# Performance work log

Hardware: AMD Instinct MI355X
Metric: run time of the kernel (lower is better)

The kernel has to match this reference:

```python
import jax, jax.numpy as jnp
import numpy as np

LEAK = 0.2
NUM_GRAPHS = 64


def _gat(h_in, src, dst, eh, W, att_src, att_dst, att_edge, lin_edge_W, bias, N):
    # PyG GATConv with edge_dim, concat=False (mean over heads)
    H, C = att_src.shape
    h = (h_in @ W).reshape(N, H, C)                      # [N,H,C]
    e = (eh @ lin_edge_W).reshape(-1, H, C)              # [Eaug,H,C]
    a_s = jnp.einsum('nhc,hc->nh', h, att_src)           # [N,H]
    a_d = jnp.einsum('nhc,hc->nh', h, att_dst)
    a_e = jnp.einsum('ehc,hc->eh', e, att_edge)          # [Eaug,H]
    score = jax.nn.leaky_relu(a_s[src] + a_d[dst] + a_e, LEAK)
    # scatter-softmax over incoming edges of each destination node
    m = jax.ops.segment_max(score, dst, num_segments=N)
    ex = jnp.exp(score - m[dst])
    den = jax.ops.segment_sum(ex, dst, num_segments=N)
    alpha = ex / den[dst]                                # [Eaug,H]
    out = jax.ops.segment_sum(alpha[:, :, None] * h[src], dst, num_segments=N)
    return out.mean(axis=1) + bias                       # concat=False -> head mean


def setup_inputs() -> dict:
    key = jax.random.key(0)
    ks = jax.random.split(key, 32)
    N, E, F, FE, HID, H, NT = 30000, 480000, 64, 16, 64, 4, 16
    Cin1 = F + HID
    s = 0.05
    d = {
        'x': jax.random.normal(ks[0], (N, F), jnp.float32),
        'edge_attr': jax.random.normal(ks[1], (E, FE), jnp.float32),
        'node_emb': jax.random.normal(ks[2], (NT, HID), jnp.float32) * s,
        'edge_W': jax.random.normal(ks[3], (FE, HID), jnp.float32) * s,
        'edge_b': jnp.zeros((HID,), jnp.float32),
        'W1': jax.random.normal(ks[4], (Cin1, H * HID), jnp.float32) * s,
        'as1': jax.random.normal(ks[5], (H, HID), jnp.float32) * s,
        'ad1': jax.random.normal(ks[6], (H, HID), jnp.float32) * s,
        'ae1': jax.random.normal(ks[7], (H, HID), jnp.float32) * s,
        'leW1': jax.random.normal(ks[8], (HID, H * HID), jnp.float32) * s,
        'b1': jnp.zeros((HID,), jnp.float32),
        'W2': jax.random.normal(ks[9], (HID, H * HID), jnp.float32) * s,
        'as2': jax.random.normal(ks[10], (H, HID), jnp.float32) * s,
        'ad2': jax.random.normal(ks[11], (H, HID), jnp.float32) * s,
        'ae2': jax.random.normal(ks[12], (H, HID), jnp.float32) * s,
        'leW2': jax.random.normal(ks[13], (HID, H * HID), jnp.float32) * s,
        'b2': jnp.zeros((HID,), jnp.float32),
        'sage_Wl': jax.random.normal(ks[14], (HID, HID), jnp.float32) * s,
        'sage_bl': jnp.zeros((HID,), jnp.float32),
        'sage_Wr': jax.random.normal(ks[15], (HID, HID), jnp.float32) * s,
        'lin1_W': jax.random.normal(ks[16], (HID, HID), jnp.float32) * s,
        'lin1_b': jnp.zeros((HID,), jnp.float32),
        'lin2_W': jax.random.normal(ks[17], (HID, HID), jnp.float32) * s,
        'lin2_b': jnp.zeros((HID,), jnp.float32),
        'tel_W': jax.random.normal(ks[18], (HID, 1), jnp.float32) * s,
        'tel_b': jnp.zeros((1,), jnp.float32),
        'comp_W': jax.random.normal(ks[19], (HID, 1), jnp.float32) * s,
        'comp_b': jnp.zeros((1,), jnp.float32),
        'pch_W': jax.random.normal(ks[20], (HID, 1), jnp.float32) * s,
        'pch_b': jnp.zeros((1,), jnp.float32),
        'edge_index': jax.random.randint(ks[21], (2, E), 0, N, jnp.int32),
        'batch': jnp.sort(jax.random.randint(ks[22], (N,), 0, NUM_GRAPHS, jnp.int32)),
        'node_type': jax.random.randint(ks[23], (N,), 0, NT, jnp.int32),
    }
    return d


def reference(x, edge_attr, node_emb, edge_W, edge_b,
              W1, as1, ad1, ae1, leW1, b1,
              W2, as2, ad2, ae2, leW2, b2,
              sage_Wl, sage_bl, sage_Wr,
              lin1_W, lin1_b, lin2_W, lin2_b,
              tel_W, tel_b, comp_W, comp_b, pch_W, pch_b,
              edge_index, batch, node_type):
    N = x.shape[0]
    src0, dst0 = edge_index[0], edge_index[1]

    h0 = jnp.concatenate([x, node_emb[node_type]], axis=-1)   # [N, F+HID]
    eh = edge_attr @ edge_W + edge_b                          # [E, HID]

    # GATConv default add_self_loops=True, fill_value='mean' on edge_attr
    loop = jnp.arange(N, dtype=src0.dtype)
    src = jnp.concatenate([src0, loop])
    dst = jnp.concatenate([dst0, loop])
    eh_aug = jnp.concatenate([eh, jnp.broadcast_to(eh.mean(axis=0), (N, eh.shape[1]))], axis=0)

    h1 = jax.nn.elu(_gat(h0, src, dst, eh_aug, W1, as1, ad1, ae1, leW1, b1, N))
    h2 = jax.nn.elu(_gat(h1, src, dst, eh_aug, W2, as2, ad2, ae2, leW2, b2, N))

    # SAGEConv: mean neighbor aggregation (src->dst) + root transform
    deg = jax.ops.segment_sum(jnp.ones_like(dst0, dtype=h2.dtype), dst0, num_segments=N)
    agg = jax.ops.segment_sum(h2[src0], dst0, num_segments=N) / jnp.clip(deg, 1.0)[:, None]
    h3 = jax.nn.elu(agg @ sage_Wl + sage_bl + h2 @ sage_Wr)

    # global mean pool per graph
    cnt = jax.ops.segment_sum(jnp.ones((N,), h3.dtype), batch, num_segments=NUM_GRAPHS)
    g = jax.ops.segment_sum(h3, batch, num_segments=NUM_GRAPHS) / jnp.clip(cnt, 1.0)[:, None]

    g = jax.nn.elu(g @ lin1_W + lin1_b)                       # dropout inactive (eval)
    g = g @ lin2_W + lin2_b
    return (g @ tel_W + tel_b, g @ comp_W + comp_b, g @ pch_W + pch_b)
```

## Files before the change

### kernel.cpp

```cpp
#include <hip/hip_runtime.h>
#include <math.h>

#define NN 30000
#define NE 480000
#define FEA 16
#define HID 64
#define NG 64
#define LEAKK 0.2f

#define S_AEL1   0
#define S_AEL2   4
#define S_KF1    16
#define S_C1     80
#define S_KF2    88
#define S_C2     152
#define S_MS1    160
#define S_MD1    672
#define S_MS2    1184
#define S_MD2    1440

__device__ __forceinline__ float eluf(float v) { return v > 0.f ? v : expm1f(v); }
__device__ __forceinline__ float leakyf(float v) { return v >= 0.f ? v : LEAKK * v; }
__device__ __forceinline__ void fma4(float4& a, float w, const float4& x) {
    a.x += w * x.x; a.y += w * x.y; a.z += w * x.z; a.w += w * x.w;
}
__device__ __forceinline__ unsigned bf16pack(float a, float b) {
    unsigned ua = __float_as_uint(a), ub = __float_as_uint(b);
    ua = (ua + 0x7FFFu + ((ua >> 16) & 1u)) >> 16;
    ub = (ub + 0x7FFFu + ((ub >> 16) & 1u)) >> 16;
    return ua | (ub << 16);
}
__device__ __forceinline__ uint2 bfpack4(float a, float b, float c, float d) {
    return make_uint2(bf16pack(a, b), bf16pack(c, d));
}
__device__ __forceinline__ float4 bf16x4(uint2 p) {
    float4 r;
    r.x = __uint_as_float(p.x << 16);
    r.y = __uint_as_float(p.x & 0xFFFF0000u);
    r.z = __uint_as_float(p.y << 16);
    r.w = __uint_as_float(p.y & 0xFFFF0000u);
    return r;
}
__device__ __forceinline__ float4 escore4(float4 a, float4 b, float4 c) {
    float4 r;
    r.x = expf(leakyf(a.x + b.x + c.x));
    r.y = expf(leakyf(a.y + b.y + c.y));
    r.z = expf(leakyf(a.z + b.z + c.z));
    r.w = expf(leakyf(a.w + b.w + c.w));
    return r;
}

__global__ __launch_bounds__(256) void cm_prepw_kernel(
    const int* __restrict__ dst, int* __restrict__ cnt, int* __restrict__ rank,
    const float* __restrict__ W1, const float* __restrict__ W2,
    const float* __restrict__ Wl, const float* __restrict__ Wr,
    const float* __restrict__ emb,
    const float* __restrict__ leW1, const float* __restrict__ aew1,
    const float* __restrict__ leW2, const float* __restrict__ aew2,
    const float* __restrict__ edge_W, const float* __restrict__ edge_b,
    const float* __restrict__ as1, const float* __restrict__ ad1,
    const float* __restrict__ as2, const float* __restrict__ ad2,
    const int* __restrict__ batch,
    float* __restrict__ WC1, float* __restrict__ WC2, float* __restrict__ B128,
    float* __restrict__ S, int* __restrict__ goff) {
    int t = threadIdx.x, bx = blockIdx.x;
    if (bx < 176) {
        int i = bx * 256 + t;
        if (i < 16384) {
            int hk = i >> 6, c = i & 63;
            int h = hk >> 6, k = hk & 63;
            WC1[i] = 0.25f * W1[k * 256 + h * 64 + c];
        } else if (i < 20480) {
            int j2 = i - 16384;
            int r2 = j2 >> 6, c = j2 & 63;
            int tau = r2 >> 2, h = r2 & 3;
            float v = 0.f;
            for (int j = 0; j < 64; j++)
                v += emb[tau * 64 + j] * W1[(64 + j) * 256 + h * 64 + c];
            WC1[i] = 0.25f * v;
        } else if (i < 36864) {
            int j = i - 20480;
            int hk = j >> 6, c = j & 63;
            int h = hk >> 6, k = hk & 63;
            WC2[j] = 0.25f * W2[k * 256 + h * 64 + c];
        } else if (i < 45056) {
            int j = i - 36864;
            int k = j >> 6, c = j & 63;
            B128[j] = (k < 64) ? Wl[k * 64 + c] : Wr[(k - 64) * 64 + c];
        }
        return;
    }
    if (bx < 178) {
        int i = (bx - 176) * 256 + t;
        int k = i >> 2, h = i & 3;
        float s = 0.f, d = 0.f;
        for (int c = 0; c < 64; c++) {
            float w = W1[k * 256 + h * 64 + c];
            s += w * as1[h * 64 + c];
            d += w * ad1[h * 64 + c];
        }
        S[S_MS1 + i] = s; S[S_MD1 + i] = d;
        return;
    }
    if (bx == 178) {
        int k = t >> 2, h = t & 3;
        float s = 0.f, d = 0.f;
        for (int c = 0; c < 64; c++) {
            float w = W2[k * 256 + h * 64 + c];
            s += w * as2[h * 64 + c];
            d += w * ad2[h * 64 + c];
        }
        S[S_MS2 + t] = s; S[S_MD2 + t] = d;
        return;
    }
    if (bx == 179) {
        __shared__ float M1s[256], M2s[256];
        {
            int k = t >> 2, h = t & 3;
            float m1 = 0.f, m2 = 0.f;
            for (int c = 0; c < 64; c++) {
                m1 += leW1[k * 256 + h * 64 + c] * aew1[h * 64 + c];
                m2 += leW2[k * 256 + h * 64 + c] * aew2[h * 64 + c];
            }
            M1s[t] = m1; M2s[t] = m2;
        }
        __syncthreads();
        if (t < 64) {
            int f = t >> 2, h = t & 3;
            float k1 = 0.f, k2 = 0.f;
            for (int k = 0; k < 64; k++) {
                k1 += edge_W[f * 64 + k] * M1s[k * 4 + h];
                k2 += edge_W[f * 64 + k] * M2s[k * 4 + h];
            }
            S[S_KF1 + t] = k1; S[S_KF2 + t] = k2;
        } else if (t < 68) {
            int h = t - 64;
            float c1 = 0.f, c2 = 0.f;
            for (int k = 0; k < 64; k++) {
                c1 += edge_b[k] * M1s[k * 4 + h];
                c2 += edge_b[k] * M2s[k * 4 + h];
            }
// ... 57 lines not shown
    int t = threadIdx.x;
    if (blockIdx.x < 118) {
        int j = blockIdx.x >> 2;
        int pref = 0;
        for (int u = 0; u < j; u++) pref += bsum[u];
        int i = blockIdx.x * 256 + t;
        if (i < NN) eoff[i] += pref;
        if (i == 0) eoff[NN] = NE;
        return;
    }
    int n0 = (blockIdx.x - 118) * 64;
    if (t < 64) {
        int n = n0 + t;
        ntS[t] = (n < NN) ? node_type[n] : 0;
    }
    for (int i = t; i < 512; i += 256) { ms[i] = S[S_MS1 + i]; md[i] = S[S_MD1 + i]; }
    __syncthreads();
    for (int i = t; i < 1024; i += 256) {
        int r = i >> 4, c4 = (i & 15) * 4;
        int n = n0 + r;
        float4 f = {0, 0, 0, 0};
        if (n < NN) f = *(const float4*)(x + (size_t)n * 64 + c4);
        *(float4*)&xt[r * 132 + c4] = f;
    }
    for (int i = t; i < 1024; i += 256) {
        int r = i >> 4, c4 = (i & 15) * 4;
        int n = n0 + r;
        float4 f = {0, 0, 0, 0};
        if (n < NN) f = *(const float4*)(node_emb + (size_t)ntS[r] * 64 + c4);
        *(float4*)&xt[r * 132 + 64 + c4] = f;
    }
    __syncthreads();
    for (int i = t; i < 2048; i += 256) {
        int r = i >> 5, u = i & 31;
        int n = n0 + r;
        if (n < NN)
            xb[(size_t)n * 32 + u] = bf16pack(xt[r * 132 + 2 * u], xt[r * 132 + 2 * u + 1]);
    }
    int r = t >> 2, h = t & 3;
    float s = 0.f, d = 0.f;
#pragma unroll 8
    for (int k = 0; k < 128; k++) {
        float xv = xt[r * 132 + k];
        s += xv * ms[k * 4 + h];
        d += xv * md[k * 4 + h];
    }
    int n = n0 + r;
    if (n < NN) { as_[n * 4 + h] = s; ad_[n * 4 + h] = d; }
}

__global__ __launch_bounds__(256) void scatter_proj_kernel(
    const int* __restrict__ src, const int* __restrict__ dst,
    const float* __restrict__ EA, const float* __restrict__ S,
    const int* __restrict__ node_type,
    const int* __restrict__ eoff, const int* __restrict__ rank,
    int* __restrict__ sep, float4* __restrict__ ae1st, float4* __restrict__ ae2st,
    float* __restrict__ Ssum) {
    __shared__ float KF1s[64], KF2s[64], Cs[8];
    __shared__ float red[32];
    int t = threadIdx.x;
    if (t < 64) { KF1s[t] = S[S_KF1 + t]; KF2s[t] = S[S_KF2 + t]; }
    else if (t < 72) { int q = t - 64; Cs[q] = (q < 4) ? S[S_C1 + q] : S[S_C2 + q - 4]; }
    __syncthreads();
    int e = blockIdx.x * 256 + t;
    int s = src[e], d = dst[e];
    float a1[4], a2[4];
#pragma unroll
    for (int h = 0; h < 4; h++) { a1[h] = Cs[h]; a2[h] = Cs[4 + h]; }
    const float4* EA4 = (const float4*)(EA + (size_t)e * FEA);
#pragma unroll
    for (int q = 0; q < 4; q++) {
        float4 v = EA4[q];
        float vv[4] = {v.x, v.y, v.z, v.w};
#pragma unroll
        for (int j = 0; j < 4; j++) {
            int f = q * 4 + j;
#pragma unroll
            for (int h = 0; h < 4; h++) {
                a1[h] += vv[j] * KF1s[f * 4 + h];
                a2[h] += vv[j] * KF2s[f * 4 + h];
            }
        }
    }
    int pos = eoff[d] + rank[e];
    sep[pos] = s | (node_type[s] << 16);
    ae1st[pos] = make_float4(a1[0], a1[1], a1[2], a1[3]);
    ae2st[pos] = make_float4(a2[0], a2[1], a2[2], a2[3]);
    float v[8] = {a1[0], a1[1], a1[2], a1[3], a2[0], a2[1], a2[2], a2[3]};
#pragma unroll
    for (int mask = 1; mask < 64; mask <<= 1)
#pragma unroll
        for (int j = 0; j < 8; j++) v[j] += __shfl_xor(v[j], mask, 64);
    int lane = t & 63, wid = t >> 6;
    if (lane == 0)
#pragma unroll
        for (int j = 0; j < 8; j++) red[wid * 8 + j] = v[j];
    __syncthreads();
    if (t < 8) atomicAdd(&Ssum[t], red[t] + red[8 + t] + red[16 + t] + red[24 + t]);
}

__global__ __launch_bounds__(256) void agg_gat1_kernel(
    const int* __restrict__ eoff, const int* __restrict__ sep,
    const float* __restrict__ ae1st, const unsigned* __restrict__ xb,
    const int* __restrict__ node_type,
    const float* __restrict__ as_, const float* __restrict__ ad_,
    const float* __restrict__ S, uint2* __restrict__ aggb) {
    int n = blockIdx.x * 4 + (threadIdx.x >> 6);
    if (n >= NN) return;
    int lane = threadIdx.x & 63;
    int sub = lane >> 4, ch = lane & 15;
    const uint2* Xb = (const uint2*)xb;
    const float4* AE4 = (const float4*)ae1st;
    const float4* AS4 = (const float4*)as_;
    float4 asn = AS4[n];
    float4 adn = ((const float4*)ad_)[n];
    float4 a0 = {0, 0, 0, 0}, a1 = a0, a2 = a0, a3 = a0, dn = a0, tw = a0;
    int b = eoff[n], e_end = eoff[n + 1];
    int nE = e_end - b;
    int i = sub;
    for (; i + 4 < nE; i += 8) {
        int p0 = b + i, p1 = p0 + 4;
        int q0 = sep[p0], q1 = sep[p1];
        int s0 = q0 & 0xFFFF, t0 = q0 >> 16;
        int s1 = q1 & 0xFFFF, t1 = q1 >> 16;
        float4 w0 = escore4(AS4[s0], adn, AE4[p0]);
        float4 w1 = escore4(AS4[s1], adn, AE4[p1]);
        float4 x0 = bf16x4(Xb[(size_t)s0 * 16 + ch]);
        float4 x1 = bf16x4(Xb[(size_t)s1 * 16 + ch]);
        fma4(a0, w0.x, x0); fma4(a1, w0.y, x0); fma4(a2, w0.z, x0); fma4(a3, w0.w, x0);
        fma4(a0, w1.x, x1); fma4(a1, w1.y, x1); fma4(a2, w1.z, x1); fma4(a3, w1.w, x1);
        dn.x += w0.x + w1.x; dn.y += w0.y + w1.y;
        dn.z += w0.z + w1.z; dn.w += w0.w + w1.w;
        if (ch == t0) { tw.x += w0.x; tw.y += w0.y; tw.z += w0.z; tw.w += w0.w; }
        if (ch == t1) { tw.x += w1.x; tw.y += w1.y; tw.z += w1.z; tw.w += w1.w; }
    }
    for (; i < nE; i += 4) {
        int p0 = b + i;
        int q0 = sep[p0];
        int s0 = q0 & 0xFFFF, t0 = q0 >> 16;
        float4 w0 = escore4(AS4[s0], adn, AE4[p0]);
        float4 x0 = bf16x4(Xb[(size_t)s0 * 16 + ch]);
        fma4(a0, w0.x, x0); fma4(a1, w0.y, x0); fma4(a2, w0.z, x0); fma4(a3, w0.w, x0);
        dn.x += w0.x; dn.y += w0.y; dn.z += w0.z; dn.w += w0.w;
        if (ch == t0) { tw.x += w0.x; tw.y += w0.y; tw.z += w0.z; tw.w += w0.w; }
    }
    if (sub == 0) {
        const float inv = 1.f / (float)NE;
        float e0 = expf(leakyf(asn.x + adn.x + S[S_AEL1 + 0] * inv));
        float e1 = expf(leakyf(asn.y + adn.y + S[S_AEL1 + 1] * inv));
        float e2 = expf(leakyf(asn.z + adn.z + S[S_AEL1 + 2] * inv));
        float e3 = expf(leakyf(asn.w + adn.w + S[S_AEL1 + 3] * inv));
        float4 xs = bf16x4(Xb[(size_t)n * 16 + ch]);
        fma4(a0, e0, xs); fma4(a1, e1, xs); fma4(a2, e2, xs); fma4(a3, e3, xs);
        dn.x += e0; dn.y += e1; dn.z += e2; dn.w += e3;
        int tn = node_type[n];
        if (ch == tn) { tw.x += e0; tw.y += e1; tw.z += e2; tw.w += e3; }
    }
#pragma unroll
    for (int mask = 16; mask < 64; mask <<= 1) {
        a0.x += __shfl_xor(a0.x, mask, 64); a0.y += __shfl_xor(a0.y, mask, 64);
        a0.z += __shfl_xor(a0.z, mask, 64); a0.w += __shfl_xor(a0.w, mask, 64);
        a1.x += __shfl_xor(a1.x, mask, 64); a1.y += __shfl_xor(a1.y, mask, 64);
        a1.z += __shfl_xor(a1.z, mask, 64); a1.w += __shfl_xor(a1.w, mask, 64);
        a2.x += __shfl_xor(a2.x, mask, 64); a2.y += __shfl_xor(a2.y, mask, 64);
        a2.z += __shfl_xor(a2.z, mask, 64); a2.w += __shfl_xor(a2.w, mask, 64);
        a3.x += __shfl_xor(a3.x, mask, 64); a3.y += __shfl_xor(a3.y, mask, 64);
        a3.z += __shfl_xor(a3.z, mask, 64); a3.w += __shfl_xor(a3.w, mask, 64);
        dn.x += __shfl_xor(dn.x, mask, 64); dn.y += __shfl_xor(dn.y, mask, 64);
        dn.z += __shfl_xor(dn.z, mask, 64); dn.w += __shfl_xor(dn.w, mask, 64);
        tw.x += __shfl_xor(tw.x, mask, 64); tw.y += __shfl_xor(tw.y, mask, 64);
        tw.z += __shfl_xor(tw.z, mask, 64); tw.w += __shfl_xor(tw.w, mask, 64);
    }
    if (sub == 0) {
        float i0 = 1.f / dn.x, i1 = 1.f / dn.y, i2 = 1.f / dn.z, i3 = 1.f / dn.w;
        uint2* A2 = aggb + (size_t)n * 80;
        A2[ch]      = bfpack4(a0.x * i0, a0.y * i0, a0.z * i0, a0.w * i0);
        A2[16 + ch] = bfpack4(a1.x * i1, a1.y * i1, a1.z * i1, a1.w * i1);
        A2[32 + ch] = bfpack4(a2.x * i2, a2.y * i2, a2.z * i2, a2.w * i2);
        A2[48 + ch] = bfpack4(a3.x * i3, a3.y * i3, a3.z * i3, a3.w * i3);
        A2[64 + ch] = bfpack4(tw.x * i0, tw.y * i1, tw.z * i2, tw.w * i3);
    }
}

__global__ __launch_bounds__(256) void agg_gat2_kernel(
    const int* __restrict__ eoff, const int* __restrict__ sep,
    const float* __restrict__ ae2st, const unsigned* __restrict__ h1b,
    const float* __restrict__ as_, const float* __restrict__ ad_,
    const float* __restrict__ S, uint2* __restrict__ aggb) {
    int n = blockIdx.x * 4 + (threadIdx.x >> 6);
    if (n >= NN) return;
    int lane = threadIdx.x & 63;
    int sub = lane >> 4, ch = lane & 15;
    const uint2* Xb = (const uint2*)h1b;
    const float4* AE4 = (const float4*)ae2st;
    const float4* AS4 = (const float4*)as_;
    float4 asn = AS4[n];
    float4 adn = ((const float4*)ad_)[n];
    float4 a0 = {0, 0, 0, 0}, a1 = a0, a2 = a0, a3 = a0, dn = a0;
    int b = eoff[n], e = eoff[n + 1];
    int nE = e - b;
    int i = sub;
    for (; i + 4 < nE; i += 8) {
        int p0 = b + i, p1 = p0 + 4;
        int q0 = sep[p0], q1 = sep[p1];
        int s0 = q0 & 0xFFFF, s1 = q1 & 0xFFFF;
        float4 w0 = escore4(AS4[s0], adn, AE4[p0]);
        float4 w1 = escore4(AS4[s1], adn, AE4[p1]);
        float4 x0 = bf16x4(Xb[(size_t)s0 * 16 + ch]);
        float4 x1 = bf16x4(Xb[(size_t)s1 * 16 + ch]);
        fma4(a0, w0.x, x0); fma4(a1, w0.y, x0); fma4(a2, w0.z, x0); fma4(a3, w0.w, x0);
        fma4(a0, w1.x, x1); fma4(a1, w1.y, x1); fma4(a2, w1.z, x1); fma4(a3, w1.w, x1);
        dn.x += w0.x + w1.x; dn.y += w0.y + w1.y;
        dn.z += w0.z + w1.z; dn.w += w0.w + w1.w;
    }
    for (; i < nE; i += 4) {
        int p0 = b + i;
        int q0 = sep[p0];
        int s0 = q0 & 0xFFFF;
        float4 w0 = escore4(AS4[s0], adn, AE4[p0]);
        float4 x0 = bf16x4(Xb[(size_t)s0 * 16 + ch]);
        fma4(a0, w0.x, x0); fma4(a1, w0.y, x0); fma4(a2, w0.z, x0); fma4(a3, w0.w, x0);
        dn.x += w0.x; dn.y += w0.y; dn.z += w0.z; dn.w += w0.w;
    }
    if (sub == 0) {
        const float inv = 1.f / (float)NE;
        float e0 = expf(leakyf(asn.x + adn.x + S[S_AEL2 + 0] * inv));
        float e1 = expf(leakyf(asn.y + adn.y + S[S_AEL2 + 1] * inv));
        float e2 = expf(leakyf(asn.z + adn.z + S[S_AEL2 + 2] * inv));
        float e3 = expf(leakyf(asn.w + adn.w + S[S_AEL2 + 3] * inv));
        float4 xs = bf16x4(Xb[(size_t)n * 16 + ch]);
        fma4(a0, e0, xs); fma4(a1, e1, xs); fma4(a2, e2, xs); fma4(a3, e3, xs);
        dn.x += e0; dn.y += e1; dn.z += e2; dn.w += e3;
    }
#pragma unroll
    for (int mask = 16; mask < 64; mask <<= 1) {
        a0.x += __shfl_xor(a0.x, mask, 64); a0.y += __shfl_xor(a0.y, mask, 64);
        a0.z += __shfl_xor(a0.z, mask, 64); a0.w += __shfl_xor(a0.w, mask, 64);
        a1.x += __shfl_xor(a1.x, mask, 64); a1.y += __shfl_xor(a1.y, mask, 64);
        a1.z += __shfl_xor(a1.z, mask, 64); a1.w += __shfl_xor(a1.w, mask, 64);
        a2.x += __shfl_xor(a2.x, mask, 64); a2.y += __shfl_xor(a2.y, mask, 64);
        a2.z += __shfl_xor(a2.z, mask, 64); a2.w += __shfl_xor(a2.w, mask, 64);
        a3.x += __shfl_xor(a3.x, mask, 64); a3.y += __shfl_xor(a3.y, mask, 64);
        a3.z += __shfl_xor(a3.z, mask, 64); a3.w += __shfl_xor(a3.w, mask, 64);
        dn.x += __shfl_xor(dn.x, mask, 64); dn.y += __shfl_xor(dn.y, mask, 64);
        dn.z += __shfl_xor(dn.z, mask, 64); dn.w += __shfl_xor(dn.w, mask, 64);
    }
    if (sub == 0) {
        float i0 = 1.f / dn.x, i1 = 1.f / dn.y, i2 = 1.f / dn.z, i3 = 1.f / dn.w;
        uint2* A2 = aggb + (size_t)n * 64;
        A2[ch]      = bfpack4(a0.x * i0, a0.y * i0, a0.z * i0, a0.w * i0);
        A2[16 + ch] = bfpack4(a1.x * i1, a1.y * i1, a1.z * i1, a1.w * i1);
        A2[32 + ch] = bfpack4(a2.x * i2, a2.y * i2, a2.z * i2, a2.w * i2);
        A2[48 + ch] = bfpack4(a3.x * i3, a3.y * i3, a3.z * i3, a3.w * i3);
    }
}

template <int K, bool DOATT>
__global__ __launch_bounds__(256) void gemm64_kernel(
    const unsigned* __restrict__ A, const float* __restrict__ B,
    const float* __restrict__ bias, float* __restrict__ out,
    unsigned* __restrict__ out16,
    const float* __restrict__ ms_g, const float* __restrict__ md_g,
    float* __restrict__ as_, float* __restrict__ ad_) {
    __shared__ float As[2][32 * 68];
    __shared__ float Bs[2][32 * 68];
    __shared__ float msS[256], mdS[256];
    int t = threadIdx.x;
    int tx = t & 15, ty = t >> 4;
    int m_base = blockIdx.x * 64;
    if (DOATT) { msS[t] = ms_g[t]; mdS[t] = md_g[t]; }
    int arow = t >> 2, ak8 = (t & 3) * 8;
    int am = m_base + arow;
    int bkr = t >> 4, bnc = (t & 15) * 4;
    const uint4* A4 = (const uint4*)A;
    const int arstride = K / 8;
    uint4 ua;
    float4 fb0, fb1;
    ua = (am < NN) ? A4[(size_t)am * arstride + (ak8 >> 3)] : make_uint4(0, 0, 0, 0);
    fb0 = *(const float4*)(B + (size_t)bkr * 64 + bnc);
    fb1 = *(const float4*)(B + (size_t)(bkr + 16) * 64 + bnc);
    {
        float4 lo = bf16x4(make_uint2(ua.x, ua.y));
        float4 hi = bf16x4(make_uint2(ua.z, ua.w));
        As[0][(ak8 + 0) * 68 + arow] = lo.x;
        As[0][(ak8 + 1) * 68 + arow] = lo.y;
        As[0][(ak8 + 2) * 68 + arow] = lo.z;
        As[0][(ak8 + 3) * 68 + arow] = lo.w;
        As[0][(ak8 + 4) * 68 + arow] = hi.x;
        As[0][(ak8 + 5) * 68 + arow] = hi.y;
        As[0][(ak8 + 6) * 68 + arow] = hi.z;
        As[0][(ak8 + 7) * 68 + arow] = hi.w;
    }
    *(float4*)&Bs[0][bkr * 68 + bnc] = fb0;
    *(float4*)&Bs[0][(bkr + 16) * 68 + bnc] = fb1;
    __syncthreads();
    float acc[4][4] = {};
    int cur = 0;
    for (int k0 = 0;; k0 += 32) {
        bool more = (k0 + 32 < K);
        if (more) {
            int kn = k0 + 32;
            ua = (am < NN) ? A4[(size_t)am * arstride + ((kn + ak8) >> 3)]
                           : make_uint4(0, 0, 0, 0);
            fb0 = *(const float4*)(B + (size_t)(kn + bkr) * 64 + bnc);
            fb1 = *(const float4*)(B + (size_t)(kn + bkr + 16) * 64 + bnc);
        }
#pragma unroll
        for (int k = 0; k < 32; k++) {
            float4 av = *(const float4*)&As[cur][k * 68 + ty * 4];
            float4 bv = *(const float4*)&Bs[cur][k * 68 + tx * 4];
            float a[4] = {av.x, av.y, av.z, av.w};
            float b[4] = {bv.x, bv.y, bv.z, bv.w};
#pragma unroll
            for (int i = 0; i < 4; i++)
#pragma unroll
                for (int j = 0; j < 4; j++) acc[i][j] += a[i] * b[j];
        }
        if (!more) break;
        int nxt = cur ^ 1;
        {
            float4 lo = bf16x4(make_uint2(ua.x, ua.y));
            float4 hi = bf16x4(make_uint2(ua.z, ua.w));
            As[nxt][(ak8 + 0) * 68 + arow] = lo.x;
            As[nxt][(ak8 + 1) * 68 + arow] = lo.y;
            As[nxt][(ak8 + 2) * 68 + arow] = lo.z;
            As[nxt][(ak8 + 3) * 68 + arow] = lo.w;
            As[nxt][(ak8 + 4) * 68 + arow] = hi.x;
            As[nxt][(ak8 + 5) * 68 + arow] = hi.y;
            As[nxt][(ak8 + 6) * 68 + arow] = hi.z;
            As[nxt][(ak8 + 7) * 68 + arow] = hi.w;
        }
        *(float4*)&Bs[nxt][bkr * 68 + bnc] = fb0;
        *(float4*)&Bs[nxt][(bkr + 16) * 68 + bnc] = fb1;
        __syncthreads();
        cur = nxt;
    }
    float4 bvv = ((const float4*)bias)[tx];
    float o[4][4];
#pragma unroll
    for (int i = 0; i < 4; i++) {
        o[i][0] = eluf(acc[i][0] + bvv.x);
        o[i][1] = eluf(acc[i][1] + bvv.y);
        o[i][2] = eluf(acc[i][2] + bvv.z);
        o[i][3] = eluf(acc[i][3] + bvv.w);
        int m = m_base + ty * 4 + i;
        if (m < NN) {
            if (out)
                *(float4*)(out + (size_t)m * 64 + tx * 4) =
                    make_float4(o[i][0], o[i][1], o[i][2], o[i][3]);
            if (out16) {
                out16[(size_t)m * 32 + tx * 2]     = bf16pack(o[i][0], o[i][1]);
                out16[(size_t)m * 32 + tx * 2 + 1] = bf16pack(o[i][2], o[i][3]);
            }
        }
    }
    if (DOATT) {
        float ps[4][4] = {}, pd[4][4] = {};
#pragma unroll
        for (int i = 0; i < 4; i++)
#pragma unroll
            for (int j = 0; j < 4; j++) {
                float v = o[i][j];
                int kk = (tx * 4 + j) * 4;
#pragma unroll
                for (int h = 0; h < 4; h++) {
                    ps[i][h] += v * msS[kk + h];
                    pd[i][h] += v * mdS[kk + h];
                }
            }
#pragma unroll
        for (int mk = 1; mk < 16; mk <<= 1) {
#pragma unroll
            for (int i = 0; i < 4; i++)
#pragma unroll
                for (int h = 0; h < 4; h++) {
                    ps[i][h] += __shfl_xor(ps[i][h], mk, 64);
                    pd[i][h] += __shfl_xor(pd[i][h], mk, 64);
                }
        }
        if (tx == 0) {
#pragma unroll
            for (int i = 0; i < 4; i++) {
                int m = m_base + ty * 4 + i;
                if (m < NN) {
                    *(float4*)(as_ + (size_t)m * 4) =
                        make_float4(ps[i][0], ps[i][1], ps[i][2], ps[i][3]);
                    *(float4*)(ad_ + (size_t)m * 4) =
                        make_float4(pd[i][0], pd[i][1], pd[i][2], pd[i][3]);
                }
            }
        }
    }
}

__global__ __launch_bounds__(256) void sage_agg3_kernel(
    const unsigned* __restrict__ h2b,
    const int* __restrict__ eoff, const int* __restrict__ sep,
    uint2* __restrict__ AB) {
    int n = blockIdx.x * 16 + (threadIdx.x >> 4);
    if (n >= NN) return;
    int l = threadIdx.x & 15;
    const uint2* Hb = (const uint2*)h2b;
    float ax = 0.f, ay = 0.f, az = 0.f, aw = 0.f;
    int b = eoff[n], e_end = eoff[n + 1];
    int idx = b;
    int stop = b + ((e_end - b) & ~7);
    if (idx < stop) {
        int sreg[8];
#pragma unroll
        for (int u = 0; u < 8; u++) sreg[u] = sep[idx + u] & 0xFFFF;
        idx += 8;
        while (true) {
            int sn[8];
            bool more = idx < stop;
            if (more) {
#pragma unroll
                for (int u = 0; u < 8; u++) sn[u] = sep[idx + u] & 0xFFFF;
            }
#pragma unroll
            for (int u = 0; u < 8; u++) {
                float4 v = bf16x4(Hb[(size_t)sreg[u] * 16 + l]);
                ax += v.x; ay += v.y; az += v.z; aw += v.w;
            }
            if (!more) break;
#pragma unroll
            for (int u = 0; u < 8; u++) sreg[u] = sn[u];
            idx += 8;
        }
    }
    for (; idx < e_end; idx++) {
        float4 v0 = bf16x4(Hb[(size_t)(sep[idx] & 0xFFFF) * 16 + l]);
        ax += v0.x; ay += v0.y; az += v0.z; aw += v0.w;
    }
    float dg = (float)(e_end - b);
    if (dg < 1.f) dg = 1.f;
    float inv = 1.f / dg;
    AB[(size_t)n * 32 + l] = bfpack4(ax * inv, ay * inv, az * inv, aw * inv);
    AB[(size_t)n * 32 + 16 + l] = Hb[(size_t)n * 16 + l];
}

__global__ __launch_bounds__(256) void pool_mlp_kernel(
// ... 48 lines not shown
    __syncthreads();
    if (t < 3) {
        float acc = 0.f;
        for (int k = 0; k < 64; k++) acc += red[t * 64 + k];
        float bb = (t == 0) ? telb[0] : ((t == 1) ? compb[0] : pchb[0]);
        out[t * 64 + gi] = acc + bb;
    }
}

extern "C" void kernel_launch(void* const* d_in, const int* in_sizes, int n_in,
                              void* d_out, int out_size, void* d_ws, size_t ws_size,
                              hipStream_t stream) {
    const float* x        = (const float*)d_in[0];
    const float* EA       = (const float*)d_in[1];
    const float* node_emb = (const float*)d_in[2];
    const float* edge_W   = (const float*)d_in[3];
    const float* edge_b   = (const float*)d_in[4];
    const float* W1       = (const float*)d_in[5];
    const float* as1      = (const float*)d_in[6];
    const float* ad1      = (const float*)d_in[7];
    const float* ae1      = (const float*)d_in[8];
    const float* leW1     = (const float*)d_in[9];
    const float* b1       = (const float*)d_in[10];
    const float* W2       = (const float*)d_in[11];
    const float* as2      = (const float*)d_in[12];
    const float* ad2      = (const float*)d_in[13];
    const float* ae2      = (const float*)d_in[14];
    const float* leW2     = (const float*)d_in[15];
    const float* b2       = (const float*)d_in[16];
    const float* sage_Wl  = (const float*)d_in[17];
    const float* sage_bl  = (const float*)d_in[18];
    const float* sage_Wr  = (const float*)d_in[19];
    const float* lin1_W   = (const float*)d_in[20];
    const float* lin1_b   = (const float*)d_in[21];
    const float* lin2_W   = (const float*)d_in[22];
    const float* lin2_b   = (const float*)d_in[23];
    const float* tel_W    = (const float*)d_in[24];
    const float* tel_b    = (const float*)d_in[25];
    const float* comp_W   = (const float*)d_in[26];
    const float* comp_b   = (const float*)d_in[27];
    const float* pch_W    = (const float*)d_in[28];
    const float* pch_b    = (const float*)d_in[29];
    const int* edge_index = (const int*)d_in[30];
    const int* batch      = (const int*)d_in[31];
    const int* node_type  = (const int*)d_in[32];
    float* outp = (float*)d_out;

    const int* srcp = edge_index;
    const int* dstp = edge_index + NE;

    float* wf = (float*)d_ws;
    constexpr size_t OFF_H3    = 0;
    constexpr size_t OFF_AGG   = OFF_H3 + (size_t)NN * 64;
    constexpr size_t OFF_AE1   = OFF_AGG + (size_t)NN * 512;
    constexpr size_t OFF_H2    = OFF_AE1 + (size_t)NE * 4;
    constexpr size_t OFF_SC    = OFF_H2 + (size_t)NN * 64;
    constexpr size_t OFF_AE2   = OFF_SC + (size_t)NE * 4;
    constexpr size_t OFF_AS    = OFF_AE2 + (size_t)NE * 4;
    constexpr size_t OFF_AD    = OFF_AS + (size_t)NN * 4;
    constexpr size_t OFF_SMALL = OFF_AD + (size_t)NN * 4;
    constexpr size_t OFF_WC1   = OFF_SMALL + 4096;
    constexpr size_t OFF_WC2   = OFF_WC1 + 20480;
    constexpr size_t OFF_B128  = OFF_WC2 + 16384;
    constexpr size_t OFF_XB    = OFF_B128 + 8192;
    constexpr size_t OFF_H1B   = OFF_XB + (size_t)NN * 32;
    constexpr size_t OFF_H2B   = OFF_H1B + (size_t)NN * 32;
    constexpr size_t F_TOTAL   = OFF_H2B + (size_t)NN * 32;

    int* wi   = (int*)(wf + F_TOTAL);
    int* cnt  = wi;
    int* rank = wi + NN;
    int* eoff = rank + NE;
    int* sep  = eoff + (NN + 2);
    int* goff = sep + NE;
    int* bsum = goff + (NG + 1);

    float* h3    = wf + OFF_H3;
    float* aggb  = wf + OFF_AGG;
    float* ae1st = wf + OFF_AE1;
    float* ae2st = wf + OFF_AE2;
    float* as_   = wf + OFF_AS;
    float* ad_   = wf + OFF_AD;
    float* S     = wf + OFF_SMALL;
    float* WC1   = wf + OFF_WC1;
    float* WC2   = wf + OFF_WC2;
    float* B128  = wf + OFF_B128;
    unsigned* xb  = (unsigned*)(wf + OFF_XB);
    unsigned* h1b = (unsigned*)(wf + OFF_H1B);
    unsigned* h2b = (unsigned*)(wf + OFF_H2B);

    hipMemsetAsync(S, 0, 16 * sizeof(float), stream);
    hipMemsetAsync(cnt, 0, NN * sizeof(int), stream);

    cm_prepw_kernel<<<181 + (NE + 255) / 256, 256, 0, stream>>>(
        dstp, cnt, rank, W1, W2, sage_Wl, sage_Wr, node_emb,
        leW1, ae1, leW2, ae2, edge_W, edge_b, as1, ad1, as2, ad2, batch,
        WC1, WC2, B128, S, goff);

    scan_blocks_kernel<<<(NN + 1023) / 1024, 1024, 0, stream>>>(cnt, eoff, bsum);
    scanadd_attn_kernel<<<118 + (NN + 63) / 64, 256, 0, stream>>>(
        bsum, eoff, x, node_emb, node_type, S, as_, ad_, xb);

    scatter_proj_kernel<<<NE / 256, 256, 0, stream>>>(
        srcp, dstp, EA, S, node_type, eoff, rank,
        sep, (float4*)ae1st, (float4*)ae2st, S);

    agg_gat1_kernel<<<(NN + 3) / 4, 256, 0, stream>>>(
        eoff, sep, ae1st, xb, node_type, as_, ad_, S, (uint2*)aggb);
    gemm64_kernel<320, true><<<(NN + 63) / 64, 256, 0, stream>>>(
        (const unsigned*)aggb, WC1, b1, nullptr, h1b, S + S_MS2, S + S_MD2, as_, ad_);

    agg_gat2_kernel<<<(NN + 3) / 4, 256, 0, stream>>>(
        eoff, sep, ae2st, h1b, as_, ad_, S, (uint2*)aggb);
    gemm64_kernel<256, false><<<(NN + 63) / 64, 256, 0, stream>>>(
        (const unsigned*)aggb, WC2, b2, nullptr, h2b, nullptr, nullptr, nullptr, nullptr);

    sage_agg3_kernel<<<(NN + 15) / 16, 256, 0, stream>>>(h2b, eoff, sep, (uint2*)aggb);
    gemm64_kernel<128, false><<<(NN + 63) / 64, 256, 0, stream>>>(
        (const unsigned*)aggb, B128, sage_bl, h3, nullptr, nullptr, nullptr, nullptr, nullptr);

    pool_mlp_kernel<<<NG, 256, 0, stream>>>(h3, goff, lin1_W, lin1_b, lin2_W, lin2_b,
                                            tel_W, tel_b, comp_W, comp_b, pch_W, pch_b, outp);
}
```

Baseline: 407.0 us.

## Use bf16 MFMA GEMMs with split hi/lo weights and precompute edge scores

Replaces the FP32 shared-memory tiled GEMMs with bf16 MFMA 16x16x32 instructions. Weights are stored transposed as hi+lo bf16 pairs so near-FP32 accuracy is kept for the B operand. Edge attention exponentials are now computed per edge in sorted order: in the scatter kernel for layer 1 and in a new score2 kernel for layer 2. This removes per-edge gather-and-exp work from the aggregation kernels, at the cost of an extra pass over the edges and a stored destination array. Also adds a layout change to bf16-per-element outputs.

```diff
diff --git a/kernel.cpp b/kernel.cpp
--- a/kernel.cpp
+++ b/kernel.cpp
@@ -19,6 +19,16 @@
 #define S_MS2    1184
 #define S_MD2    1440
 
+#define BT1H 0
+#define BT1L 20480
+#define BT2H 40960
+#define BT2L 57344
+#define BT3H 73728
+#define BT3L 81920
+
+typedef __attribute__((ext_vector_type(8))) short short8;
+typedef __attribute__((ext_vector_type(4))) float f32x4;
+
 __device__ __forceinline__ float eluf(float v) { return v > 0.f ? v : expm1f(v); }
 __device__ __forceinline__ float leakyf(float v) { return v >= 0.f ? v : LEAKK * v; }
 __device__ __forceinline__ void fma4(float4& a, float w, const float4& x) {
@@ -29,6 +39,13 @@
     ua = (ua + 0x7FFFu + ((ua >> 16) & 1u)) >> 16;
     ub = (ub + 0x7FFFu + ((ub >> 16) & 1u)) >> 16;
     return ua | (ub << 16);
+}
+__device__ __forceinline__ unsigned short bf1(float v) {
+    unsigned u = __float_as_uint(v);
+    return (unsigned short)((u + 0x7FFFu + ((u >> 16) & 1u)) >> 16);
+}
+__device__ __forceinline__ float bf1tof(unsigned short h) {
+    return __uint_as_float(((unsigned)h) << 16);
 }
 __device__ __forceinline__ uint2 bfpack4(float a, float b, float c, float d) {
     return make_uint2(bf16pack(a, b), bf16pack(c, d));
@@ -61,32 +78,44 @@
     const float* __restrict__ as1, const float* __restrict__ ad1,
     const float* __restrict__ as2, const float* __restrict__ ad2,
     const int* __restrict__ batch,
-    float* __restrict__ WC1, float* __restrict__ WC2, float* __restrict__ B128,
+    unsigned short* __restrict__ BT,
     float* __restrict__ S, int* __restrict__ goff) {
     int t = threadIdx.x, bx = blockIdx.x;
     if (bx < 176) {
         int i = bx * 256 + t;
+        float v = 0.f;
+        int dsti = -1;
         if (i < 16384) {
-            int hk = i >> 6, c = i & 63;
-            int h = hk >> 6, k = hk & 63;
-            WC1[i] = 0.25f * W1[k * 256 + h * 64 + c];
+            int kk = i >> 6, c = i & 63;
+            int h = kk >> 6, k = kk & 63;
+            v = 0.25f * W1[k * 256 + h * 64 + c];
+            dsti = BT1H + c * 320 + kk;
         } else if (i < 20480) {
             int j2 = i - 16384;
             int r2 = j2 >> 6, c = j2 & 63;
             int tau = r2 >> 2, h = r2 & 3;
-            float v = 0.f;
+            float acc = 0.f;
             for (int j = 0; j < 64; j++)
-                v += emb[tau * 64 + j] * W1[(64 + j) * 256 + h * 64 + c];
-            WC1[i] = 0.25f * v;
+                acc += emb[tau * 64 + j] * W1[(64 + j) * 256 + h * 64 + c];
+            v = 0.25f * acc;
+            dsti = BT1H + c * 320 + 256 + r2;
         } else if (i < 36864) {
             int j = i - 20480;
-            int hk = j >> 6, c = j & 63;
-            int h = hk >> 6, k = hk & 63;
-            WC2[j] = 0.25f * W2[k * 256 + h * 64 + c];
+            int kk = j >> 6, c = j & 63;
+            int h = kk >> 6, k = kk & 63;
+            v = 0.25f * W2[k * 256 + h * 64 + c];
+            dsti = BT2H + c * 256 + kk;
         } else if (i < 45056) {
             int j = i - 36864;
             int k = j >> 6, c = j & 63;
-            B128[j] = (k < 64) ? Wl[k * 64 + c] : Wr[(k - 64) * 64 + c];
+            v = (k < 64) ? Wl[k * 64 + c] : Wr[(k - 64) * 64 + c];
+            dsti = BT3H + c * 128 + k;
+        }
+        if (dsti >= 0) {
+            unsigned short hi = bf1(v);
+            unsigned short lo = bf1(v - bf1tof(hi));
+            BT[dsti] = hi;
+            BT[dsti + 20480 - ((dsti >= BT2H) ? ((dsti >= BT3H) ? 12288 : 4096) : 0)] = lo;
         }
         return;
     }
@@ -250,9 +279,11 @@
 __global__ __launch_bounds__(256) void scatter_proj_kernel(
     const int* __restrict__ src, const int* __restrict__ dst,
     const float* __restrict__ EA, const float* __restrict__ S,
+    const float* __restrict__ as_, const float* __restrict__ ad_,
     const int* __restrict__ node_type,
     const int* __restrict__ eoff, const int* __restrict__ rank,
-    int* __restrict__ sep, float4* __restrict__ ae1st, float4* __restrict__ ae2st,
+    int* __restrict__ sep, int* __restrict__ dsrt,
+    float4* __restrict__ sc1st, float4* __restrict__ ae2st,
     float* __restrict__ Ssum) {
     __shared__ float KF1s[64], KF2s[64], Cs[8];
     __shared__ float red[32];
@@ -282,7 +313,10 @@
     }
     int pos = eoff[d] + rank[e];
     sep[pos] = s | (node_type[s] << 16);
-    ae1st[pos] = make_float4(a1[0], a1[1], a1[2], a1[3]);
+    dsrt[pos] = d;
+    float4 asv = ((const float4*)as_)[s];
+    float4 adv = ((const float4*)ad_)[d];
+    sc1st[pos] = escore4(asv, adv, make_float4(a1[0], a1[1], a1[2], a1[3]));
     ae2st[pos] = make_float4(a2[0], a2[1], a2[2], a2[3]);
     float v[8] = {a1[0], a1[1], a1[2], a1[3], a2[0], a2[1], a2[2], a2[3]};
 #pragma unroll
@@ -297,9 +331,19 @@
     if (t < 8) atomicAdd(&Ssum[t], red[t] + red[8 + t] + red[16 + t] + red[24 + t]);
 }
 
+__global__ __launch_bounds__(256) void score2_kernel(
+    const int* __restrict__ sep, const int* __restrict__ dsrt,
+    const float* __restrict__ as_, const float* __restrict__ ad_,
+    float4* __restrict__ ae2st) {
+    int p = blockIdx.x * 256 + threadIdx.x;
+    int s = sep[p] & 0xFFFF;
+    int d = dsrt[p];
+    ae2st[p] = escore4(((const float4*)as_)[s], ((const float4*)ad_)[d], ae2st[p]);
+}
+
 __global__ __launch_bounds__(256) void agg_gat1_kernel(
     const int* __restrict__ eoff, const int* __restrict__ sep,
-    const float* __restrict__ ae1st, const unsigned* __restrict__ xb,
+    const float* __restrict__ scs, const unsigned* __restrict__ xb,
     const int* __restrict__ node_type,
     const float* __restrict__ as_, const float* __restrict__ ad_,
     const float* __restrict__ S, uint2* __restrict__ aggb) {
@@ -308,9 +352,8 @@
     int lane = threadIdx.x & 63;
     int sub = lane >> 4, ch = lane & 15;
     const uint2* Xb = (const uint2*)xb;
-    const float4* AE4 = (const float4*)ae1st;
-    const float4* AS4 = (const float4*)as_;
-    float4 asn = AS4[n];
+    const float4* W4 = (const float4*)scs;
+    float4 asn = ((const float4*)as_)[n];
     float4 adn = ((const float4*)ad_)[n];
     float4 a0 = {0, 0, 0, 0}, a1 = a0, a2 = a0, a3 = a0, dn = a0, tw = a0;
     int b = eoff[n], e_end = eoff[n + 1];
@@ -321,8 +364,7 @@
         int q0 = sep[p0], q1 = sep[p1];
         int s0 = q0 & 0xFFFF, t0 = q0 >> 16;
         int s1 = q1 & 0xFFFF, t1 = q1 >> 16;
-        float4 w0 = escore4(AS4[s0], adn, AE4[p0]);
-        float4 w1 = escore4(AS4[s1], adn, AE4[p1]);
+        float4 w0 = W4[p0], w1 = W4[p1];
         float4 x0 = bf16x4(Xb[(size_t)s0 * 16 + ch]);
         float4 x1 = bf16x4(Xb[(size_t)s1 * 16 + ch]);
         fma4(a0, w0.x, x0); fma4(a1, w0.y, x0); fma4(a2, w0.z, x0); fma4(a3, w0.w, x0);
@@ -336,7 +378,7 @@
         int p0 = b + i;
         int q0 = sep[p0];
         int s0 = q0 & 0xFFFF, t0 = q0 >> 16;
-        float4 w0 = escore4(AS4[s0], adn, AE4[p0]);
+        float4 w0 = W4[p0];
         float4 x0 = bf16x4(Xb[(size_t)s0 * 16 + ch]);
         fma4(a0, w0.x, x0); fma4(a1, w0.y, x0); fma4(a2, w0.z, x0); fma4(a3, w0.w, x0);
         dn.x += w0.x; dn.y += w0.y; dn.z += w0.z; dn.w += w0.w;
@@ -382,7 +424,7 @@
 
 __global__ __launch_bounds__(256) void agg_gat2_kernel(
     const int* __restrict__ eoff, const int* __restrict__ sep,
-    const float* __restrict__ ae2st, const unsigned* __restrict__ h1b,
+    const float* __restrict__ w2s, const unsigned* __restrict__ h1b,
     const float* __restrict__ as_, const float* __restrict__ ad_,
     const float* __restrict__ S, uint2* __restrict__ aggb) {
     int n = blockIdx.x * 4 + (threadIdx.x >> 6);
@@ -390,9 +432,8 @@
     int lane = threadIdx.x & 63;
     int sub = lane >> 4, ch = lane & 15;
     const uint2* Xb = (const uint2*)h1b;
-    const float4* AE4 = (const float4*)ae2st;
-    const float4* AS4 = (const float4*)as_;
-    float4 asn = AS4[n];
+    const float4* W4 = (const float4*)w2s;
+    float4 asn = ((const float4*)as_)[n];
     float4 adn = ((const float4*)ad_)[n];
     float4 a0 = {0, 0, 0, 0}, a1 = a0, a2 = a0, a3 = a0, dn = a0;
     int b = eoff[n], e = eoff[n + 1];
@@ -400,10 +441,8 @@
     int i = sub;
     for (; i + 4 < nE; i += 8) {
         int p0 = b + i, p1 = p0 + 4;
-        int q0 = sep[p0], q1 = sep[p1];
-        int s0 = q0 & 0xFFFF, s1 = q1 & 0xFFFF;
-        float4 w0 = escore4(AS4[s0], adn, AE4[p0]);
-        float4 w1 = escore4(AS4[s1], adn, AE4[p1]);
+        int s0 = sep[p0] & 0xFFFF, s1 = sep[p1] & 0xFFFF;
+        float4 w0 = W4[p0], w1 = W4[p1];
         float4 x0 = bf16x4(Xb[(size_t)s0 * 16 + ch]);
         float4 x1 = bf16x4(Xb[(size_t)s1 * 16 + ch]);
         fma4(a0, w0.x, x0); fma4(a1, w0.y, x0); fma4(a2, w0.z, x0); fma4(a3, w0.w, x0);
@@ -413,9 +452,8 @@
     }
     for (; i < nE; i += 4) {
         int p0 = b + i;
-        int q0 = sep[p0];
-        int s0 = q0 & 0xFFFF;
-        float4 w0 = escore4(AS4[s0], adn, AE4[p0]);
+        int s0 = sep[p0] & 0xFFFF;
+        float4 w0 = W4[p0];
         float4 x0 = bf16x4(Xb[(size_t)s0 * 16 + ch]);
         fma4(a0, w0.x, x0); fma4(a1, w0.y, x0); fma4(a2, w0.z, x0); fma4(a3, w0.w, x0);
         dn.x += w0.x; dn.y += w0.y; dn.z += w0.z; dn.w += w0.w;
@@ -454,137 +492,85 @@
 }
 
 template <int K, bool DOATT>
-__global__ __launch_bounds__(256) void gemm64_kernel(
-    const unsigned* __restrict__ A, const float* __restrict__ B,
+__global__ __launch_bounds__(256) void gemm_mfma_kernel(
+    const unsigned* __restrict__ A, const unsigned short* __restrict__ bth,
+    const unsigned short* __restrict__ btl,
     const float* __restrict__ bias, float* __restrict__ out,
-    unsigned* __restrict__ out16,
+    unsigned short* __restrict__ out16,
     const float* __restrict__ ms_g, const float* __restrict__ md_g,
     float* __restrict__ as_, float* __restrict__ ad_) {
-    __shared__ float As[2][32 * 68];
-    __shared__ float Bs[2][32 * 68];
-    __shared__ float msS[256], mdS[256];
     int t = threadIdx.x;
-    int tx = t & 15, ty = t >> 4;
-    int m_base = blockIdx.x * 64;
-    if (DOATT) { msS[t] = ms_g[t]; mdS[t] = md_g[t]; }
-    int arow = t >> 2, ak8 = (t & 3) * 8;
-    int am = m_base + arow;
-    int bkr = t >> 4, bnc = (t & 15) * 4;
-    const uint4* A4 = (const uint4*)A;
-    const int arstride = K / 8;
-    uint4 ua;
-    float4 fb0, fb1;
-    ua = (am < NN) ? A4[(size_t)am * arstride + (ak8 >> 3)] : make_uint4(0, 0, 0, 0);
-    fb0 = *(const float4*)(B + (size_t)bkr * 64 + bnc);
-    fb1 = *(const float4*)(B + (size_t)(bkr + 16) * 64 + bnc);
-    {
-        float4 lo = bf16x4(make_uint2(ua.x, ua.y));
-        float4 hi = bf16x4(make_uint2(ua.z, ua.w));
-        As[0][(ak8 + 0) * 68 + arow] = lo.x;
-        As[0][(ak8 + 1) * 68 + arow] = lo.y;
-        As[0][(ak8 + 2) * 68 + arow] = lo.z;
-        As[0][(ak8 + 3) * 68 + arow] = lo.w;
-        As[0][(ak8 + 4) * 68 + arow] = hi.x;
-        As[0][(ak8 + 5) * 68 + arow] = hi.y;
-        As[0][(ak8 + 6) * 68 + arow] = hi.z;
-        As[0][(ak8 + 7) * 68 + arow] = hi.w;
-    }
-    *(float4*)&Bs[0][bkr * 68 + bnc] = fb0;
-    *(float4*)&Bs[0][(bkr + 16) * 68 + bnc] = fb1;
-    __syncthreads();
-    float acc[4][4] = {};
-    int cur = 0;
-    for (int k0 = 0;; k0 += 32) {
-        bool more = (k0 + 32 < K);
-        if (more) {
-            int kn = k0 + 32;
-            ua = (am < NN) ? A4[(size_t)am * arstride + ((kn + ak8) >> 3)]
-                           : make_uint4(0, 0, 0, 0);
-            fb0 = *(const float4*)(B + (size_t)(kn + bkr) * 64 + bnc);
-            fb1 = *(const float4*)(B + (size_t)(kn + bkr + 16) * 64 + bnc);
-        }
-#pragma unroll
-        for (int k = 0; k < 32; k++) {
-            float4 av = *(const float4*)&As[cur][k * 68 + ty * 4];
-            float4 bv = *(const float4*)&Bs[cur][k * 68 + tx * 4];
-            float a[4] = {av.x, av.y, av.z, av.w};
-            float b[4] = {bv.x, bv.y, bv.z, bv.w};
-#pragma unroll
-            for (int i = 0; i < 4; i++)
-#pragma unroll
-                for (int j = 0; j < 4; j++) acc[i][j] += a[i] * b[j];
-        }
-        if (!more) break;
-        int nxt = cur ^ 1;
-        {
-            float4 lo = bf16x4(make_uint2(ua.x, ua.y));
-            float4 hi = bf16x4(make_uint2(ua.z, ua.w));
-            As[nxt][(ak8 + 0) * 68 + arow] = lo.x;
-            As[nxt][(ak8 + 1) * 68 + arow] = lo.y;
-            As[nxt][(ak8 + 2) * 68 + arow] = lo.z;
-            As[nxt][(ak8 + 3) * 68 + arow] = lo.w;
-            As[nxt][(ak8 + 4) * 68 + arow] = hi.x;
-            As[nxt][(ak8 + 5) * 68 + arow] = hi.y;
-            As[nxt][(ak8 + 6) * 68 + arow] = hi.z;
-            As[nxt][(ak8 + 7) * 68 + arow] = hi.w;
-        }
-        *(float4*)&Bs[nxt][bkr * 68 + bnc] = fb0;
-        *(float4*)&Bs[nxt][(bkr + 16) * 68 + bnc] = fb1;
-        __syncthreads();
-        cur = nxt;
-    }
-    float4 bvv = ((const float4*)bias)[tx];
-    float o[4][4];
-#pragma unroll
-    for (int i = 0; i < 4; i++) {
-        o[i][0] = eluf(acc[i][0] + bvv.x);
-        o[i][1] = eluf(acc[i][1] + bvv.y);
-        o[i][2] = eluf(acc[i][2] + bvv.z);
-        o[i][3] = eluf(acc[i][3] + bvv.w);
-        int m = m_base + ty * 4 + i;
-        if (m < NN) {
-            if (out)
-                *(float4*)(out + (size_t)m * 64 + tx * 4) =
-                    make_float4(o[i][0], o[i][1], o[i][2], o[i][3]);
-            if (out16) {
-                out16[(size_t)m * 32 + tx * 2]     = bf16pack(o[i][0], o[i][1]);
-                out16[(size_t)m * 32 + tx * 2 + 1] = bf16pack(o[i][2], o[i][3]);
-            }
-        }
-    }
+    int w = t >> 6, l = t & 63;
+    int lr = l & 15, lg = l >> 4;
+    int m0 = blockIdx.x * 64 + w * 16;
+    int am = m0 + lr;
+    bool av = am < NN;
+    const short8* Arow = (const short8*)A + (size_t)am * (K / 8);
+    short8 zz = {0, 0, 0, 0, 0, 0, 0, 0};
+    f32x4 acc[4];
+#pragma unroll
+    for (int ct = 0; ct < 4; ct++) acc[ct] = (f32x4){0.f, 0.f, 0.f, 0.f};
+#pragma unroll
+    for (int k0 = 0; k0 < K; k0 += 32) {
+        short8 a = av ? Arow[(k0 >> 3) + lg] : zz;
+#pragma unroll
+        for (int ct = 0; ct < 4; ct++) {
+            int bo = (ct * 16 + lr) * K + k0 + lg * 8;
+            short8 bh = *(const short8*)(bth + bo);
+            short8 bl = *(const short8*)(btl + bo);
+            acc[ct] = __builtin_amdgcn_mfma_f32_16x16x32_bf16(a, bh, acc[ct], 0, 0, 0);
+            acc[ct] = __builtin_amdgcn_mfma_f32_16x16x32_bf16(a, bl, acc[ct], 0, 0, 0);
+        }
+    }
+    f32x4 ps[4], pd[4];
     if (DOATT) {
-        float ps[4][4] = {}, pd[4][4] = {};
-#pragma unroll
-        for (int i = 0; i < 4; i++)
-#pragma unroll
-            for (int j = 0; j < 4; j++) {
-                float v = o[i][j];
-                int kk = (tx * 4 + j) * 4;
-#pragma unroll
-                for (int h = 0; h < 4; h++) {
-                    ps[i][h] += v * msS[kk + h];
-                    pd[i][h] += v * mdS[kk + h];
-                }
-            }
-#pragma unroll
-        for (int mk = 1; mk < 16; mk <<= 1) {
-#pragma unroll
-            for (int i = 0; i < 4; i++)
-#pragma unroll
-                for (int h = 0; h < 4; h++) {
-                    ps[i][h] += __shfl_xor(ps[i][h], mk, 64);
-                    pd[i][h] += __shfl_xor(pd[i][h], mk, 64);
-                }
-        }
-        if (tx == 0) {
-#pragma unroll
-            for (int i = 0; i < 4; i++) {
-                int m = m_base + ty * 4 + i;
+#pragma unroll
+        for (int r = 0; r < 4; r++) {
+            ps[r] = (f32x4){0.f, 0.f, 0.f, 0.f};
+            pd[r] = (f32x4){0.f, 0.f, 0.f, 0.f};
+        }
+    }
+#pragma unroll
+    for (int ct = 0; ct < 4; ct++) {
+        int col = ct * 16 + lr;
+        float bv = bias[col];
+        f32x4 ms4, md4;
+        if (DOATT) {
+            ms4 = ((const f32x4*)ms_g)[col];
+            md4 = ((const f32x4*)md_g)[col];
+        }
+#pragma unroll
+        for (int r = 0; r < 4; r++) {
+            int m = m0 + lg * 4 + r;
+            float o = eluf(acc[ct][r] + bv);
+            if (m < NN) {
+                if (out) out[(size_t)m * 64 + col] = o;
+                if (out16) out16[(size_t)m * 64 + col] = bf1(o);
+            }
+            if (DOATT) { ps[r] += o * ms4; pd[r] += o * md4; }
+        }
+    }
+    if (DOATT) {
+#pragma unroll
+        for (int mk = 1; mk < 16; mk <<= 1)
+#pragma unroll
+            for (int r = 0; r < 4; r++) {
+                ps[r][0] += __shfl_xor(ps[r][0], mk, 64);
+                ps[r][1] += __shfl_xor(ps[r][1], mk, 64);
+                ps[r][2] += __shfl_xor(ps[r][2], mk, 64);
+                ps[r][3] += __shfl_xor(ps[r][3], mk, 64);
+                pd[r][0] += __shfl_xor(pd[r][0], mk, 64);
+                pd[r][1] += __shfl_xor(pd[r][1], mk, 64);
+                pd[r][2] += __shfl_xor(pd[r][2], mk, 64);
+                pd[r][3] += __shfl_xor(pd[r][3], mk, 64);
+            }
+        if (lr == 0) {
+#pragma unroll
+            for (int r = 0; r < 4; r++) {
+                int m = m0 + lg * 4 + r;
                 if (m < NN) {
-                    *(float4*)(as_ + (size_t)m * 4) =
-                        make_float4(ps[i][0], ps[i][1], ps[i][2], ps[i][3]);
-                    *(float4*)(ad_ + (size_t)m * 4) =
-                        make_float4(pd[i][0], pd[i][1], pd[i][2], pd[i][3]);
+                    *(f32x4*)(as_ + (size_t)m * 4) = ps[r];
+                    *(f32x4*)(ad_ + (size_t)m * 4) = pd[r];
                 }
             }
         }
@@ -739,17 +725,15 @@
     float* wf = (float*)d_ws;
     constexpr size_t OFF_H3    = 0;
     constexpr size_t OFF_AGG   = OFF_H3 + (size_t)NN * 64;
-    constexpr size_t OFF_AE1   = OFF_AGG + (size_t)NN * 512;
-    constexpr size_t OFF_H2    = OFF_AE1 + (size_t)NE * 4;
+    constexpr size_t OFF_SC1   = OFF_AGG + (size_t)NN * 512;
+    constexpr size_t OFF_H2    = OFF_SC1 + (size_t)NE * 4;
     constexpr size_t OFF_SC    = OFF_H2 + (size_t)NN * 64;
     constexpr size_t OFF_AE2   = OFF_SC + (size_t)NE * 4;
     constexpr size_t OFF_AS    = OFF_AE2 + (size_t)NE * 4;
     constexpr size_t OFF_AD    = OFF_AS + (size_t)NN * 4;
     constexpr size_t OFF_SMALL = OFF_AD + (size_t)NN * 4;
-    constexpr size_t OFF_WC1   = OFF_SMALL + 4096;
-    constexpr size_t OFF_WC2   = OFF_WC1 + 20480;
-    constexpr size_t OFF_B128  = OFF_WC2 + 16384;
-    constexpr size_t OFF_XB    = OFF_B128 + 8192;
+    constexpr size_t OFF_BT    = OFF_SMALL + 4096;
+    constexpr size_t OFF_XB    = OFF_BT + 45056;
     constexpr size_t OFF_H1B   = OFF_XB + (size_t)NN * 32;
     constexpr size_t OFF_H2B   = OFF_H1B + (size_t)NN * 32;
     constexpr size_t F_TOTAL   = OFF_H2B + (size_t)NN * 32;
@@ -759,22 +743,21 @@
     int* rank = wi + NN;
     int* eoff = rank + NE;
     int* sep  = eoff + (NN + 2);
-    int* goff = sep + NE;
+    int* dsrt = sep + NE;
+    int* goff = dsrt + NE;
     int* bsum = goff + (NG + 1);
 
     float* h3    = wf + OFF_H3;
     float* aggb  = wf + OFF_AGG;
-    float* ae1st = wf + OFF_AE1;
+    float* sc1st = wf + OFF_SC1;
     float* ae2st = wf + OFF_AE2;
     float* as_   = wf + OFF_AS;
     float* ad_   = wf + OFF_AD;
     float* S     = wf + OFF_SMALL;
-    float* WC1   = wf + OFF_WC1;
-    float* WC2   = wf + OFF_WC2;
-    float* B128  = wf + OFF_B128;
+    unsigned short* BT = (unsigned short*)(wf + OFF_BT);
     unsigned* xb  = (unsigned*)(wf + OFF_XB);
-    unsigned* h1b = (unsigned*)(wf + OFF_H1B);
-    unsigned* h2b = (unsigned*)(wf + OFF_H2B);
+    unsigned short* h1b = (unsigned short*)(wf + OFF_H1B);
+    unsigned short* h2b = (unsigned short*)(wf + OFF_H2B);
 
     hipMemsetAsync(S, 0, 16 * sizeof(float), stream);
     hipMemsetAsync(cnt, 0, NN * sizeof(int), stream);
@@ -782,29 +765,34 @@
     cm_prepw_kernel<<<181 + (NE + 255) / 256, 256, 0, stream>>>(
         dstp, cnt, rank, W1, W2, sage_Wl, sage_Wr, node_emb,
         leW1, ae1, leW2, ae2, edge_W, edge_b, as1, ad1, as2, ad2, batch,
-        WC1, WC2, B128, S, goff);
+        BT, S, goff);
 
     scan_blocks_kernel<<<(NN + 1023) / 1024, 1024, 0, stream>>>(cnt, eoff, bsum);
     scanadd_attn_kernel<<<118 + (NN + 63) / 64, 256, 0, stream>>>(
         bsum, eoff, x, node_emb, node_type, S, as_, ad_, xb);
 
     scatter_proj_kernel<<<NE / 256, 256, 0, stream>>>(
-        srcp, dstp, EA, S, node_type, eoff, rank,
-        sep, (float4*)ae1st, (float4*)ae2st, S);
+        srcp, dstp, EA, S, as_, ad_, node_type, eoff, rank,
+        sep, dsrt, (float4*)sc1st, (float4*)ae2st, S);
 
     agg_gat1_kernel<<<(NN + 3) / 4, 256, 0, stream>>>(
-        eoff, sep, ae1st, xb, node_type, as_, ad_, S, (uint2*)aggb);
-    gemm64_kernel<320, true><<<(NN + 63) / 64, 256, 0, stream>>>(
-        (const unsigned*)aggb, WC1, b1, nullptr, h1b, S + S_MS2, S + S_MD2, as_, ad_);
-
+        eoff, sep, sc1st, xb, node_type, as_, ad_, S, (uint2*)aggb);
+    gemm_mfma_kernel<320, true><<<(NN + 63) / 64, 256, 0, stream>>>(
+        (const unsigned*)aggb, BT + BT1H, BT + BT1L, b1, nullptr, h1b,
+        S + S_MS2, S + S_MD2, as_, ad_);
+
+    score2_kernel<<<NE / 256, 256, 0, stream>>>(sep, dsrt, as_, ad_, (float4*)ae2st);
     agg_gat2_kernel<<<(NN + 3) / 4, 256, 0, stream>>>(
-        eoff, sep, ae2st, h1b, as_, ad_, S, (uint2*)aggb);
-    gemm64_kernel<256, false><<<(NN + 63) / 64, 256, 0, stream>>>(
-        (const unsigned*)aggb, WC2, b2, nullptr, h2b, nullptr, nullptr, nullptr, nullptr);
-
-    sage_agg3_kernel<<<(NN + 15) / 16, 256, 0, stream>>>(h2b, eoff, sep, (uint2*)aggb);
-    gemm64_kernel<128, false><<<(NN + 63) / 64, 256, 0, stream>>>(
-        (const unsigned*)aggb, B128, sage_bl, h3, nullptr, nullptr, nullptr, nullptr, nullptr);
+        eoff, sep, ae2st, (const unsigned*)h1b, as_, ad_, S, (uint2*)aggb);
+    gemm_mfma_kernel<256, false><<<(NN + 63) / 64, 256, 0, stream>>>(
+        (const unsigned*)aggb, BT + BT2H, BT + BT2L, b2, nullptr, h2b,
+        nullptr, nullptr, nullptr, nullptr);
+
+    sage_agg3_kernel<<<(NN + 15) / 16, 256, 0, stream>>>(
+        (const unsigned*)h2b, eoff, sep, (uint2*)aggb);
+    gemm_mfma_kernel<128, false><<<(NN + 63) / 64, 256, 0, stream>>>(
+        (const unsigned*)aggb, BT + BT3H, BT + BT3L, sage_bl, h3, nullptr,
+        nullptr, nullptr, nullptr, nullptr);
 
     pool_mlp_kernel<<<NG, 256, 0, stream>>>(h3, goff, lin1_W, lin1_b, lin2_W, lin2_b,
                                             tel_W, tel_b, comp_W, comp_b, pch_W, pch_b, outp);
```

Result: faster. 386.0 us (-5.2%).
